# Performance work log

Hardware: AMD Instinct MI355X
Metric: run time of the kernel (lower is better)

## Reference

```python
import jax, jax.numpy as jnp
import numpy as np
from jax import lax

B, L, D, F, K = 16, 1024, 384, 1536, 3
MAX_DUR = 10          # clamp on per-token duration (makes output length static)
T_OUT = L * MAX_DUR   # padded expanded length
ALPHA = 1.0
EPS = 1e-5


def conv1d_same(x_ncl, w, b):
    # x_ncl: [B, Cin, L], w: [Cout, Cin, K]
    y = lax.conv_general_dilated(x_ncl, w, window_strides=(1,), padding='SAME',
                                 dimension_numbers=('NCH', 'OIH', 'NCH'))
    return y + b[None, :, None]


def conv_block(x, wA, bA, wB, bB):
    # x: [B, L, D] -> Conv(D->F) ReLU Conv(F->D) ReLU -> [B, L, D]
    h = x.transpose(0, 2, 1)
    h = jax.nn.relu(conv1d_same(h, wA, bA))
    h = jax.nn.relu(conv1d_same(h, wB, bB))
    return h.transpose(0, 2, 1)


def layernorm(x, g, b):
    mu = jnp.mean(x, axis=-1, keepdims=True)
    var = jnp.var(x, axis=-1, keepdims=True)
    return (x - mu) * lax.rsqrt(var + EPS) * g + b


def setup_inputs() -> dict:
    key = jax.random.key(0)
    ks = jax.random.split(key, 8)
    s = 0.02
    return {
        'y': jax.random.normal(ks[0], (B, L, D), jnp.float32),
        'token_lengths': jax.random.randint(ks[1], (B,), 1, L + 1).astype(jnp.int32),
        'w1a': jax.random.normal(ks[2], (F, D, K), jnp.float32) * s,
        'b1a': jnp.zeros((F,), jnp.float32),
        'w1b': jax.random.normal(ks[3], (D, F, K), jnp.float32) * s,
        'b1b': jnp.zeros((D,), jnp.float32),
        'g1': jnp.ones((D,), jnp.float32),
        'be1': jnp.zeros((D,), jnp.float32),
        'w2a': jax.random.normal(ks[4], (F, D, K), jnp.float32) * s,
        'b2a': jnp.zeros((F,), jnp.float32),
        'w2b': jax.random.normal(ks[5], (D, F, K), jnp.float32) * s,
        'b2b': jnp.zeros((D,), jnp.float32),
        'g2': jnp.ones((D,), jnp.float32),
        'be2': jnp.zeros((D,), jnp.float32),
        'wl': jax.random.normal(ks[6], (D, 1), jnp.float32) * s,
        'bl': jnp.zeros((1,), jnp.float32),
    }


def reference(y, token_lengths, w1a, b1a, w1b, b1b, g1, be1,
              w2a, b2a, w2b, b2b, g2, be2, wl, bl):
    # DurationPredictor (eval mode: dropout is identity)
    h = conv_block(y, w1a, b1a, w1b, b1b)
    h = layernorm(h, g1, be1)
    h = conv_block(h, w2a, b2a, w2b, b2b)
    h = layernorm(h, g2, be2)
    preds = h @ wl + bl                      # [B, L, 1]

    # lengths = round(alpha * exp(preds)), masked to valid tokens, clamped
    lns = jnp.round(ALPHA * jnp.exp(preds[..., 0]))
    lns = jnp.clip(lns, 0, MAX_DUR).astype(jnp.int32)        # [B, L]
    mask = jnp.arange(L)[None, :] < token_lengths[:, None]
    lns = jnp.where(mask, lns, 0)

    # ragged repeat_interleave + pad, fully vectorized:
    # output frame t maps to token idx = searchsorted(cumsum(lns), t, 'right')
    csum = jnp.cumsum(lns, axis=1)                            # [B, L]
    totals = csum[:, -1]                                      # [B]
    t = jnp.arange(T_OUT, dtype=jnp.int32)
    idx = jax.vmap(lambda c: jnp.searchsorted(c, t, side='right'))(csum)  # [B, T_OUT]
    idx = jnp.minimum(idx, L - 1)
    gathered = jnp.take_along_axis(y, idx[..., None], axis=1)  # [B, T_OUT, D]
    valid = t[None, :] < totals[:, None]
    enlarged = jnp.where(valid[..., None], gathered, 0.0)
    return enlarged, totals
```

## Files before the change

kernel.cpp:

```cpp
#include <hip/hip_runtime.h>
#include <hip/hip_bf16.h>

#define BB 16
#define LL 1024
#define DD 384
#define FF 1536
#define KK 3
#define T_OUT 10240
#define MAX_DUR 10

#define PADL 1026
#define LO_SCALE 2048.0f
#define LO_INV   4.8828125e-4f

typedef _Float16 f16x8 __attribute__((ext_vector_type(8)));
typedef float    f32x4 __attribute__((ext_vector_type(4)));

__device__ __forceinline__ void gll16(const void* g, void* l) {
    __builtin_amdgcn_global_load_lds(
        (const __attribute__((address_space(1))) void*)g,
        (__attribute__((address_space(3))) void*)l, 16, 0, 0);
}

__device__ __forceinline__ void split_write(float v, _Float16* hi, _Float16* lo, size_t off) {
    _Float16 h = (_Float16)v;
    hi[off] = h;
    lo[off] = (_Float16)((v - (float)h) * LO_SCALE);
}

__device__ __forceinline__ float split_read(const _Float16* hi, const _Float16* lo, size_t off) {
    return (float)hi[off] + (float)lo[off] * LO_INV;
}

__global__ void prep_w(const float* __restrict__ w1a, const float* __restrict__ w1b,
                       const float* __restrict__ w2a, const float* __restrict__ w2b,
                       _Float16* __restrict__ base) {
    const int total = FF * 3 * DD;
    int id = blockIdx.x * 256 + threadIdx.x;
    int which = id / total;
    int rid = id - which * total;
    if (which >= 4) return;
    const float* w; _Float16 *hi, *lo; int I;
    const size_t WN = (size_t)FF * DD * KK;
    if (which == 0)      { w = w1a; I = DD; hi = base;          lo = base + WN; }
    else if (which == 1) { w = w1b; I = FF; hi = base + 2 * WN; lo = base + 3 * WN; }
    else if (which == 2) { w = w2a; I = DD; hi = base + 4 * WN; lo = base + 5 * WN; }
    else                 { w = w2b; I = FF; hi = base + 6 * WN; lo = base + 7 * WN; }
    int e = rid & 7;
    int lane = (rid >> 3) & 63;
    int rest = rid >> 9;
    int nKT = (3 * I) >> 5;
    int ktl = rest % nKT;
    int ot = rest / nKT;
    int o = ot * 16 + (lane & 15);
    int koff = ((lane >> 4) << 3) + e;
    int kseg = ktl % 3;
    int i = (ktl / 3) * 32 + koff;
    float v = w[(o * I + i) * 3 + kseg];
    split_write(v, hi, lo, rid);
}

__global__ void prep_y(const float* __restrict__ y, _Float16* __restrict__ shi,
                       _Float16* __restrict__ slo, _Float16* __restrict__ h1hi,
                       _Float16* __restrict__ h1lo) {
    const int SNc = BB * PADL * DD;
    int id = blockIdx.x * 256 + threadIdx.x;
    if (id < SNc) {
        int d = id % DD;
        int r = id / DD;
        int b = r / PADL;
        int lr = r - b * PADL;
        float v = 0.f;
        if (lr >= 1 && lr <= LL) v = y[((size_t)(b << 10) + (lr - 1)) * DD + d];
        split_write(v, shi, slo, id);
        return;
    }
    int id2 = id - SNc;
    if (id2 >= BB * 2 * FF) return;
    int b = id2 / (2 * FF);
    int rem = id2 - b * 2 * FF;
    int row = (rem / FF) ? (PADL - 1) : 0;
    int c = rem % FF;
    size_t off = (size_t)(b * PADL + row) * FF + c;
    h1hi[off] = (_Float16)0.f;
    h1lo[off] = (_Float16)0.f;
}

__global__ __launch_bounds__(256, 2) void gemm_split(
        const _Float16* __restrict__ Ahi, const _Float16* __restrict__ Alo,
        const _Float16* __restrict__ WfH, const _Float16* __restrict__ WfL,
        const float* __restrict__ bias,
        _Float16* __restrict__ Ohi, _Float16* __restrict__ Olo,
        size_t halfStride,
        int Cin, int Cout, int nKTper, int nN, int blocksPerHalf, int doRelu) {
    __shared__ _Float16 lds_h[16384];
    const int tid = threadIdx.x;
    const int lane = tid & 63;
    const int w = tid >> 6;
    const int lm = lane & 15, lq = lane >> 4;
    const int nKTfull = (3 * Cin) >> 5;
    const int half = blockIdx.x / blocksPerHalf;
    const int t2in = blockIdx.x - half * blocksPerHalf;
    const int xcd = t2in & 7;
    const int t2 = t2in >> 3;
    const int g  = t2 / (4 * nN);
    const int r  = t2 - g * (4 * nN);
    const int n_t = r >> 2;
    const int mi  = r & 3;
    const int m_t = ((g * 4 + mi) << 3) + xcd;
    const int m0 = m_t << 7;
    const int n0 = n_t << 7;
    const int b = m0 >> 10;
    const int l0 = m0 & 1023;
    const int rowBase = b * PADL + l0;
    const int wm = (w >> 1) * 64, wn = (w & 1) * 64;
    const int ktBegin = half * nKTper;
    const int ktEnd = ktBegin + nKTper;

    f32x4 accM[4][4], accC[4][4];
    const f32x4 zz = {0.f, 0.f, 0.f, 0.f};
    #pragma unroll
    for (int i = 0; i < 4; ++i)
        #pragma unroll
        for (int jj = 0; jj < 4; ++jj) { accM[i][jj] = zz; accC[i][jj] = zz; }

    auto stageA = [&](int kt, int nxt) {
        int kseg = kt % 3;
        int d0 = (kt / 3) << 5;
        #pragma unroll
        for (int it = 0; it < 2; ++it) {
            int s = (w * 2 + it) * 64 + lane;
            int p = s >> 3, sl = s & 7;
            int t = sl ^ (p & 7);
            int m = p * 2 + (t >> 2);
            int k8 = t & 3;
            size_t aoff = (size_t)(rowBase + m + kseg) * Cin + d0 + k8 * 8;
            _Float16* lbase = lds_h + nxt * 8192 + (size_t)(w * 2 + it) * 512;
            gll16(Ahi + aoff, lbase);
            gll16(Alo + aoff, lbase + 4096);
        }
    };

    stageA(ktBegin, 0);
    for (int kt = ktBegin; kt < ktEnd; ++kt) {
        const int cur = (kt - ktBegin) & 1;
        __syncthreads();
        f16x8 bH[4], bL[4];
        #pragma unroll
        for (int jj = 0; jj < 4; ++jj) {
            int ntg = (n0 + wn + jj * 16) >> 4;
            size_t boff = (((size_t)ntg * nKTfull + kt) * 64 + lane) * 8;
            bH[jj] = *(const f16x8*)(WfH + boff);
            bL[jj] = *(const f16x8*)(WfL + boff);
        }
        if (kt + 1 < ktEnd) stageA(kt + 1, cur ^ 1);
        const _Float16* lb = lds_h + cur * 8192;
        f16x8 aH[4], aL[4];
        #pragma unroll
        for (int i = 0; i < 4; ++i) {
            int m = wm + i * 16 + lm;
            int p = m >> 1;
            int sl = (((m & 1) << 2) | lq) ^ (p & 7);
            int off = p * 64 + sl * 8;
            aH[i] = *(const f16x8*)(lb + off);
            aL[i] = *(const f16x8*)(lb + 4096 + off);
        }
        #pragma unroll
        for (int jj = 0; jj < 4; ++jj)
            #pragma unroll
            for (int i = 0; i < 4; ++i) {
                accM[i][jj] = __builtin_amdgcn_mfma_f32_16x16x32_f16(aH[i], bH[jj], accM[i][jj], 0, 0, 0);
                accC[i][jj] = __builtin_amdgcn_mfma_f32_16x16x32_f16(aH[i], bL[jj], accC[i][jj], 0, 0, 0);
                accC[i][jj] = __builtin_amdgcn_mfma_f32_16x16x32_f16(aL[i], bH[jj], accC[i][jj], 0, 0, 0);
            }
    }
    _Float16* oh = Ohi + (size_t)half * halfStride;
    _Float16* ol = Olo + (size_t)half * halfStride;
    #pragma unroll
    for (int i = 0; i < 4; ++i)
        #pragma unroll
        for (int jj = 0; jj < 4; ++jj) {
            int n_g = n0 + wn + jj * 16 + lm;
            float bv = doRelu ? bias[n_g] : 0.f;
            #pragma unroll
            for (int rr = 0; rr < 4; ++rr) {
                int l = l0 + wm + i * 16 + lq * 4 + rr;
                float v = accM[i][jj][rr] + accC[i][jj][rr] * LO_INV + bv;
                if (doRelu) v = fmaxf(v, 0.f);
                size_t off = (size_t)(b * PADL + 1 + l) * Cout + n_g;
                split_write(v, oh, ol, off);
            }
        }
}

__global__ __launch_bounds__(128) void reduce_ln_k(
        const _Float16* __restrict__ Pbase, size_t halfStride,
        _Float16* __restrict__ Shi, _Float16* __restrict__ Slo,
        const float* __restrict__ bias, const float* __restrict__ g,
        const float* __restrict__ be) {
    const int row = blockIdx.x;
    const int b = row >> 10, l = row & 1023;
    const size_t SNc = (size_t)BB * PADL * DD;
    const size_t base = (size_t)(b * PADL + 1 + l) * DD;
    const int tid = threadIdx.x;
    float v0 = bias[tid], v1 = bias[tid + 128], v2 = bias[tid + 256];
    #pragma unroll
    for (int h = 0; h < 4; ++h) {
        const _Float16* ph = Pbase + (size_t)h * halfStride;
        const _Float16* pl = ph + SNc;
        v0 += split_read(ph, pl, base + tid);
        v1 += split_read(ph, pl, base + tid + 128);
        v2 += split_read(ph, pl, base + tid + 256);
    }
    v0 = fmaxf(v0, 0.f); v1 = fmaxf(v1, 0.f); v2 = fmaxf(v2, 0.f);

    __shared__ float sh[2];
    float s = v0 + v1 + v2;
    #pragma unroll
    for (int o = 32; o > 0; o >>= 1) s += __shfl_down(s, o, 64);
    if ((tid & 63) == 0) sh[tid >> 6] = s;
    __syncthreads();
    float mu = (sh[0] + sh[1]) * (1.f / DD);
    __syncthreads();
    float d0 = v0 - mu, d1 = v1 - mu, d2 = v2 - mu;
    float q = d0 * d0 + d1 * d1 + d2 * d2;
    #pragma unroll
    for (int o = 32; o > 0; o >>= 1) q += __shfl_down(q, o, 64);
    if ((tid & 63) == 0) sh[tid >> 6] = q;
    __syncthreads();
    float var = (sh[0] + sh[1]) * (1.f / DD);
    float rs = rsqrtf(var + 1e-5f);
    split_write(d0 * rs * g[tid] + be[tid], Shi, Slo, base + tid);
    split_write(d1 * rs * g[tid + 128] + be[tid + 128], Shi, Slo, base + tid + 128);
    split_write(d2 * rs * g[tid + 256] + be[tid + 256], Shi, Slo, base + tid + 256);
}

__global__ __launch_bounds__(128) void reduce_ln_pred_k(
        const _Float16* __restrict__ Pbase, size_t halfStride,
        const float* __restrict__ bias, const float* __restrict__ g,
        const float* __restrict__ be, const float* __restrict__ wl,
        const float* __restrict__ bl, const int* __restrict__ token_lengths,
        int* __restrict__ lns) {
    const int row = blockIdx.x;
    const int b = row >> 10, l = row & 1023;
    const size_t SNc = (size_t)BB * PADL * DD;
    const size_t base = (size_t)(b * PADL + 1 + l) * DD;
    const int tid = threadIdx.x;
    float v0 = bias[tid], v1 = bias[tid + 128], v2 = bias[tid + 256];
    #pragma unroll
    for (int h = 0; h < 4; ++h) {
        const _Float16* ph = Pbase + (size_t)h * halfStride;
        const _Float16* pl = ph + SNc;
        v0 += split_read(ph, pl, base + tid);
        v1 += split_read(ph, pl, base + tid + 128);
        v2 += split_read(ph, pl, base + tid + 256);
    }
    v0 = fmaxf(v0, 0.f); v1 = fmaxf(v1, 0.f); v2 = fmaxf(v2, 0.f);

    __shared__ float sh[2];
    float s = v0 + v1 + v2;
    #pragma unroll
    for (int o = 32; o > 0; o >>= 1) s += __shfl_down(s, o, 64);
    if ((tid & 63) == 0) sh[tid >> 6] = s;
    __syncthreads();
    float mu = (sh[0] + sh[1]) * (1.f / DD);
    __syncthreads();
    float d0 = v0 - mu, d1 = v1 - mu, d2 = v2 - mu;
    float q = d0 * d0 + d1 * d1 + d2 * d2;
    #pragma unroll
    for (int o = 32; o > 0; o >>= 1) q += __shfl_down(q, o, 64);
    if ((tid & 63) == 0) sh[tid >> 6] = q;
    __syncthreads();
    float var = (sh[0] + sh[1]) * (1.f / DD);
    float rs = rsqrtf(var + 1e-5f);
    __syncthreads();
    float p = (d0 * rs * g[tid]       + be[tid])       * wl[tid]
            + (d1 * rs * g[tid + 128] + be[tid + 128]) * wl[tid + 128]
            + (d2 * rs * g[tid + 256] + be[tid + 256]) * wl[tid + 256];
    #pragma unroll
    for (int o = 32; o > 0; o >>= 1) p += __shfl_down(p, o, 64);
    if ((tid & 63) == 0) sh[tid >> 6] = p;
    __syncthreads();
    if (tid == 0) {
        float pred = sh[0] + sh[1] + bl[0];
        float e = expf(pred);
        float r = rintf(e);
        r = fminf(fmaxf(r, 0.f), (float)MAX_DUR);
        int v = (int)r;
        if (l >= token_lengths[b]) v = 0;
        lns[row] = v;
    }
}

__global__ __launch_bounds__(1024) void cumsum_k(
        const int* __restrict__ lns, int* __restrict__ csum,
        float* __restrict__ totals_out) {
    __shared__ int s[1024];
    const int b = blockIdx.x, tid = threadIdx.x;
    s[tid] = lns[(b << 10) + tid];
    __syncthreads();
    #pragma unroll
    for (int o = 1; o < 1024; o <<= 1) {
        int t = (tid >= o) ? s[tid - o] : 0;
        __syncthreads();
        s[tid] += t;
        __syncthreads();
    }
    csum[(b << 10) + tid] = s[tid];
    if (tid == 1023) totals_out[b] = (float)s[1023];
}

__global__ __launch_bounds__(256) void idx_k(
        const int* __restrict__ csum, int* __restrict__ idxArr) {
    int id = blockIdx.x * 256 + threadIdx.x;
    if (id >= BB * T_OUT) return;
    int b = id / T_OUT, t = id - b * T_OUT;
    const int* c = csum + (b << 10);
    int total = c[1023];
    int r = -1;
    if (t < total) {
        int lo = 0, hi = 1024;
        while (lo < hi) {
            int mid = (lo + hi) >> 1;
            if (c[mid] <= t) lo = mid + 1; else hi = mid;
        }
        r = min(lo, LL - 1);
    }
    idxArr[id] = r;
}

__global__ __launch_bounds__(256) void gather_k(
        const float* __restrict__ y, const int* __restrict__ idxArr,
        float* __restrict__ out) {
    int gid = blockIdx.x * 256 + threadIdx.x;
    int c4 = gid % 96;
    int rest = gid / 96;
    int t = rest % T_OUT;
    int b = rest / T_OUT;
    int r = idxArr[b * T_OUT + t];
    float4 v = make_float4(0.f, 0.f, 0.f, 0.f);
    if (r >= 0) v = *(const float4*)(y + ((size_t)((b << 10) + r)) * DD + (c4 << 2));
    *(float4*)(out + ((size_t)b * T_OUT + t) * DD + (c4 << 2)) = v;
}

extern "C" void kernel_launch(void* const* d_in, const int* in_sizes, int n_in,
                              void* d_out, int out_size, void* d_ws, size_t ws_size,
                              hipStream_t stream) {
    const float* y   = (const float*)d_in[0];
    const int*   tok = (const int*)d_in[1];
    const float* w1a = (const float*)d_in[2];
    const float* b1a = (const float*)d_in[3];
    const float* w1b = (const float*)d_in[4];
    const float* b1b = (const float*)d_in[5];
    const float* g1  = (const float*)d_in[6];
    const float* be1 = (const float*)d_in[7];
    const float* w2a = (const float*)d_in[8];
    const float* b2a = (const float*)d_in[9];
    const float* w2b = (const float*)d_in[10];
    const float* b2b = (const float*)d_in[11];
    const float* g2  = (const float*)d_in[12];
    const float* be2 = (const float*)d_in[13];
    const float* wl  = (const float*)d_in[14];
    const float* bl  = (const float*)d_in[15];

    float* out = (float*)d_out;

    const size_t WN   = (size_t)FF * DD * KK;
    const size_t SN   = (size_t)BB * PADL * DD;
    const size_t H1N  = (size_t)BB * PADL * FF;
    _Float16* wsh = (_Float16*)d_ws;
    _Float16* Wh1a = wsh;            _Float16* Wl1a = Wh1a + WN;
    _Float16* Wh1b = Wl1a + WN;      _Float16* Wl1b = Wh1b + WN;
    _Float16* Wh2a = Wl1b + WN;      _Float16* Wl2a = Wh2a + WN;
    _Float16* Wh2b = Wl2a + WN;      _Float16* Wl2b = Wh2b + WN;
    _Float16* Shi  = Wl2b + WN;      _Float16* Slo  = Shi + SN;
    _Float16* H1hi = Slo + SN;       _Float16* H1lo = H1hi + H1N;
    int* lns    = (int*)(H1lo + H1N);
    int* csum   = lns + BB * LL;
    int* idxArr = csum + BB * LL;

    _Float16* Pbase = (_Float16*)d_out;
    const size_t halfStride = 2 * SN;

    const int M = BB * LL;

    prep_w<<<(4 * FF * 3 * DD) / 256, 256, 0, stream>>>(w1a, w1b, w2a, w2b, wsh);
    prep_y<<<(int)((SN + BB * 2 * FF + 255) / 256), 256, 0, stream>>>(y, Shi, Slo, H1hi, H1lo);

    const int ffBlocks = (M / 128) * (FF / 128);
    const int ddBlocksPerHalf = (M / 128) * (DD / 128);

    gemm_split<<<ffBlocks, 256, 0, stream>>>(
        Shi, Slo, Wh1a, Wl1a, b1a, H1hi, H1lo, 0,
        DD, FF, (3 * DD) >> 5, FF / 128, ffBlocks, 1);
    gemm_split<<<4 * ddBlocksPerHalf, 256, 0, stream>>>(
        H1hi, H1lo, Wh1b, Wl1b, b1b, Pbase, Pbase + SN, halfStride,
        FF, DD, ((3 * FF) >> 5) / 4, DD / 128, ddBlocksPerHalf, 0);
    reduce_ln_k<<<M, 128, 0, stream>>>(Pbase, halfStride, Shi, Slo, b1b, g1, be1);

    gemm_split<<<ffBlocks, 256, 0, stream>>>(
        Shi, Slo, Wh2a, Wl2a, b2a, H1hi, H1lo, 0,
        DD, FF, (3 * DD) >> 5, FF / 128, ffBlocks, 1);
    gemm_split<<<4 * ddBlocksPerHalf, 256, 0, stream>>>(
        H1hi, H1lo, Wh2b, Wl2b, b2b, Pbase, Pbase + SN, halfStride,
        FF, DD, ((3 * FF) >> 5) / 4, DD / 128, ddBlocksPerHalf, 0);
    reduce_ln_pred_k<<<M, 128, 0, stream>>>(Pbase, halfStride, b2b, g2, be2, wl, bl, tok, lns);

    cumsum_k<<<BB, 1024, 0, stream>>>(lns, csum, out + (size_t)BB * T_OUT * DD);
    idx_k<<<(BB * T_OUT + 255) / 256, 256, 0, stream>>>(csum, idxArr);
    {
        long long n = (long long)BB * T_OUT * 96;
        gather_k<<<(int)((n + 255) / 256), 256, 0, stream>>>(y, idxArr, out);
    }
}
```

Before: 1.051 ms.

## Stage one halo A tile per channel group and reuse it across kernel taps

The conv-as-GEMM kernel now stages one 130-row A tile per 32-channel group in LDS, instead of a separate 128-row tile for each of the three kernel taps. Each tap reads the same tile shifted by one row. This cuts global-to-LDS A traffic and barriers by about three times. In exchange it drops the XOR swizzle, which risks LDS bank conflicts, and uses plain loads for the two halo rows.

```diff
diff --git a/kernel.cpp b/kernel.cpp
--- a/kernel.cpp
+++ b/kernel.cpp
@@ -93,7 +93,7 @@
         _Float16* __restrict__ Ohi, _Float16* __restrict__ Olo,
         size_t halfStride,
         int Cin, int Cout, int nKTper, int nN, int blocksPerHalf, int doRelu) {
-    __shared__ _Float16 lds_h[16384];
+    __shared__ _Float16 lds_h[17408];
     const int tid = threadIdx.x;
     const int lane = tid & 63;
     const int w = tid >> 6;
@@ -114,8 +114,8 @@
     const int l0 = m0 & 1023;
     const int rowBase = b * PADL + l0;
     const int wm = (w >> 1) * 64, wn = (w & 1) * 64;
-    const int ktBegin = half * nKTper;
-    const int ktEnd = ktBegin + nKTper;
+    const int gBegin = (half * nKTper) / 3;
+    const int nGroups = nKTper / 3;
 
     f32x4 accM[4][4], accC[4][4];
     const f32x4 zz = {0.f, 0.f, 0.f, 0.f};
@@ -124,55 +124,62 @@
         #pragma unroll
         for (int jj = 0; jj < 4; ++jj) { accM[i][jj] = zz; accC[i][jj] = zz; }
 
-    auto stageA = [&](int kt, int nxt) {
-        int kseg = kt % 3;
-        int d0 = (kt / 3) << 5;
+    auto stageGroup = [&](int grp, int ph) {
+        int d0 = grp << 5;
+        _Float16* baseHi = lds_h + ph * 8704;
+        _Float16* baseLo = baseHi + 4352;
         #pragma unroll
         for (int it = 0; it < 2; ++it) {
-            int s = (w * 2 + it) * 64 + lane;
-            int p = s >> 3, sl = s & 7;
-            int t = sl ^ (p & 7);
-            int m = p * 2 + (t >> 2);
-            int k8 = t & 3;
-            size_t aoff = (size_t)(rowBase + m + kseg) * Cin + d0 + k8 * 8;
-            _Float16* lbase = lds_h + nxt * 8192 + (size_t)(w * 2 + it) * 512;
-            gll16(Ahi + aoff, lbase);
-            gll16(Alo + aoff, lbase + 4096);
+            int s = it * 256 + tid;
+            int row = s >> 2;
+            int c16 = s & 3;
+            size_t aoff = (size_t)(rowBase + row) * Cin + d0 + c16 * 8;
+            gll16(Ahi + aoff, baseHi + (size_t)s * 8);
+            gll16(Alo + aoff, baseLo + (size_t)s * 8);
+        }
+        if (tid < 8) {
+            int row = 128 + (tid >> 2);
+            int c16 = tid & 3;
+            size_t aoff = (size_t)(rowBase + row) * Cin + d0 + c16 * 8;
+            int s = row * 4 + c16;
+            *(f16x8*)(lds_h + ph * 8704 + (size_t)s * 8)        = *(const f16x8*)(Ahi + aoff);
+            *(f16x8*)(lds_h + ph * 8704 + 4352 + (size_t)s * 8) = *(const f16x8*)(Alo + aoff);
         }
     };
 
-    stageA(ktBegin, 0);
-    for (int kt = ktBegin; kt < ktEnd; ++kt) {
-        const int cur = (kt - ktBegin) & 1;
+    stageGroup(gBegin, 0);
+    int ph = 0;
+    for (int gi = 0; gi < nGroups; ++gi) {
         __syncthreads();
-        f16x8 bH[4], bL[4];
+        if (gi + 1 < nGroups) stageGroup(gBegin + gi + 1, ph ^ 1);
+        const _Float16* hb = lds_h + ph * 8704;
+        const _Float16* lb2 = hb + 4352;
         #pragma unroll
-        for (int jj = 0; jj < 4; ++jj) {
-            int ntg = (n0 + wn + jj * 16) >> 4;
-            size_t boff = (((size_t)ntg * nKTfull + kt) * 64 + lane) * 8;
-            bH[jj] = *(const f16x8*)(WfH + boff);
-            bL[jj] = *(const f16x8*)(WfL + boff);
-        }
-        if (kt + 1 < ktEnd) stageA(kt + 1, cur ^ 1);
-        const _Float16* lb = lds_h + cur * 8192;
-        f16x8 aH[4], aL[4];
-        #pragma unroll
-        for (int i = 0; i < 4; ++i) {
-            int m = wm + i * 16 + lm;
-            int p = m >> 1;
-            int sl = (((m & 1) << 2) | lq) ^ (p & 7);
-            int off = p * 64 + sl * 8;
-            aH[i] = *(const f16x8*)(lb + off);
-            aL[i] = *(const f16x8*)(lb + 4096 + off);
-        }
-        #pragma unroll
-        for (int jj = 0; jj < 4; ++jj)
+        for (int kseg = 0; kseg < 3; ++kseg) {
+            const int kt = (gBegin + gi) * 3 + kseg;
+            f16x8 bH[4], bL[4];
+            #pragma unroll
+            for (int jj = 0; jj < 4; ++jj) {
+                int ntg = (n0 + wn + jj * 16) >> 4;
+                size_t boff = (((size_t)ntg * nKTfull + kt) * 64 + lane) * 8;
+                bH[jj] = *(const f16x8*)(WfH + boff);
+                bL[jj] = *(const f16x8*)(WfL + boff);
+            }
             #pragma unroll
             for (int i = 0; i < 4; ++i) {
-                accM[i][jj] = __builtin_amdgcn_mfma_f32_16x16x32_f16(aH[i], bH[jj], accM[i][jj], 0, 0, 0);
-                accC[i][jj] = __builtin_amdgcn_mfma_f32_16x16x32_f16(aH[i], bL[jj], accC[i][jj], 0, 0, 0);
-                accC[i][jj] = __builtin_amdgcn_mfma_f32_16x16x32_f16(aL[i], bH[jj], accC[i][jj], 0, 0, 0);
+                int row = wm + i * 16 + lm + kseg;
+                int off = row * 32 + lq * 8;
+                f16x8 aH = *(const f16x8*)(hb + off);
+                f16x8 aL = *(const f16x8*)(lb2 + off);
+                #pragma unroll
+                for (int jj = 0; jj < 4; ++jj) {
+                    accM[i][jj] = __builtin_amdgcn_mfma_f32_16x16x32_f16(aH, bH[jj], accM[i][jj], 0, 0, 0);
+                    accC[i][jj] = __builtin_amdgcn_mfma_f32_16x16x32_f16(aH, bL[jj], accC[i][jj], 0, 0, 0);
+                    accC[i][jj] = __builtin_amdgcn_mfma_f32_16x16x32_f16(aL, bH[jj], accC[i][jj], 0, 0, 0);
+                }
             }
+        }
+        ph ^= 1;
     }
     _Float16* oh = Ohi + (size_t)half * halfStride;
     _Float16* ol = Olo + (size_t)half * halfStride;
```

After: 1.103 ms. +4.9%, slower.
